# Kernel tuning notes

Measured on AMD Instinct MI355X. Metric: run time of the kernel, lower is better.

The kernel has to match this reference:

```python
import jax, jax.numpy as jnp
import numpy as np

N_EMBD = 1024
N_HEAD = 16
HEAD_DIM = N_EMBD // N_HEAD


def setup_inputs() -> dict:
    key = jax.random.key(0)
    ks = jax.random.split(key, 9)
    s = 1.0 / np.sqrt(N_EMBD)
    x = jax.random.normal(ks[0], (2, 2048, N_EMBD), dtype=jnp.float32)
    # PyTorch Linear weights stored as (out_features, in_features)
    Wq = jax.random.uniform(ks[1], (N_EMBD, N_EMBD), jnp.float32, -s, s)
    bq = jax.random.uniform(ks[2], (N_EMBD,), jnp.float32, -s, s)
    Wk = jax.random.uniform(ks[3], (N_EMBD, N_EMBD), jnp.float32, -s, s)
    bk = jax.random.uniform(ks[4], (N_EMBD,), jnp.float32, -s, s)
    Wv = jax.random.uniform(ks[5], (N_EMBD, N_EMBD), jnp.float32, -s, s)
    bv = jax.random.uniform(ks[6], (N_EMBD,), jnp.float32, -s, s)
    Wfc = jax.random.uniform(ks[7], (N_EMBD, N_EMBD), jnp.float32, -s, s)
    bfc = jax.random.uniform(ks[8], (N_EMBD,), jnp.float32, -s, s)
    return {"x": x, "Wq": Wq, "bq": bq, "Wk": Wk, "bk": bk,
            "Wv": Wv, "bv": bv, "Wfc": Wfc, "bfc": bfc}


def reference(x, Wq, bq, Wk, bk, Wv, bv, Wfc, bfc):
    B, S, _ = x.shape

    def proj(W, b):
        y = jnp.einsum('bsd,ed->bse', x, W) + b  # Linear: x @ W.T + b
        return y.reshape(B, S, N_HEAD, HEAD_DIM).transpose(0, 2, 1, 3)  # [B,H,S,Dh]

    q = proj(Wq, bq)
    k = proj(Wk, bk)
    v = proj(Wv, bv)
    scores = jnp.einsum('bhqd,bhkd->bhqk', q, k) / jnp.sqrt(jnp.float32(HEAD_DIM))
    weights = jax.nn.softmax(scores, axis=-1)  # [B,H,S,S]
    out = jnp.einsum('bhqk,bhkd->bhqd', weights, v)
    out = out.transpose(0, 2, 1, 3).reshape(B, S, N_EMBD)
    out = jnp.einsum('bsd,ed->bse', out, Wfc) + bfc
    return (out, weights)
```

## Files before the change

### kernel.cpp

```cpp
#include <hip/hip_runtime.h>
#include <hip/hip_bf16.h>
#include <stdint.h>


typedef __attribute__((ext_vector_type(8))) short bf16x8;
typedef __attribute__((ext_vector_type(4))) short bf16x4;
typedef __attribute__((ext_vector_type(4))) float f32x4;

#define MFMA16(a, b, c) __builtin_amdgcn_mfma_f32_16x16x32_bf16(a, b, c, 0, 0, 0)

__device__ __forceinline__ short f2bf(float x) {
  uint32_t u = __builtin_bit_cast(uint32_t, x);
  u += 0x7FFFu + ((u >> 16) & 1u);
  return (short)(u >> 16);
}

__device__ __forceinline__ uint32_t cvtpk_bf16(float lo, float hi) {
  uint32_t r;
  asm("v_cvt_pk_bf16_f32 %0, %1, %2" : "=v"(r) : "v"(lo), "v"(hi));
  return r;
}

__device__ __forceinline__ void gload16(const void* g, void* l) {
  __builtin_amdgcn_global_load_lds((const __attribute__((address_space(1))) uint32_t*)g,
                                   (__attribute__((address_space(3))) uint32_t*)l, 16, 0, 0);
}

__global__ __launch_bounds__(256) void cvt_k(const float* __restrict__ src,
                                             short* __restrict__ dst, int n4) {
  int i = blockIdx.x * 256 + threadIdx.x;
  if (i < n4) {
    f32x4 v = *(const f32x4*)(src + (size_t)i * 4);
    bf16x4 o;
    o[0] = f2bf(v[0]); o[1] = f2bf(v[1]); o[2] = f2bf(v[2]); o[3] = f2bf(v[3]);
    *(bf16x4*)(dst + (size_t)i * 4) = o;
  }
}

template <int EPI>
__global__ __launch_bounds__(256) void gemm_k(
    const short* __restrict__ A, const short* __restrict__ B,
    const float* __restrict__ bq, const float* __restrict__ bk,
    const float* __restrict__ bv,
    short* __restrict__ Qb, short* __restrict__ Kb, short* __restrict__ Vt,
    float* __restrict__ Fout) {
  const int K = 1024;
  __shared__ short sA[128 * 32];
  __shared__ short sB[128 * 32];
  const int tid = threadIdx.x;
  const int w = tid >> 6, lane = tid & 63;
  const int wr = w >> 1, wc = w & 1;
  const int lrow = lane & 15, lk = (lane >> 4) * 8;
  const int tileM = blockIdx.x * 128, tileN = blockIdx.y * 128;

  f32x4 acc[4][4];
#pragma unroll
  for (int i = 0; i < 4; ++i)
#pragma unroll
    for (int j = 0; j < 4; ++j) acc[i][j] = (f32x4){0.f, 0.f, 0.f, 0.f};

  for (int k0 = 0; k0 < K; k0 += 32) {
#pragma unroll
    for (int i = 0; i < 2; ++i) {
      int u = (w * 2 + i) * 64 + lane;
      int row = u >> 2, c8 = (u & 3) * 8;
      gload16(A + (size_t)(tileM + row) * K + k0 + c8, (short*)sA + (w * 2 + i) * 512);
      gload16(B + (size_t)(tileN + row) * K + k0 + c8, (short*)sB + (w * 2 + i) * 512);
    }
    __syncthreads();
    bf16x8 af[4], bfr[4];
#pragma unroll
    for (int mi = 0; mi < 4; ++mi)
      af[mi] = *(const bf16x8*)&sA[(wr * 64 + mi * 16 + lrow) * 32 + lk];
#pragma unroll
    for (int ni = 0; ni < 4; ++ni)
      bfr[ni] = *(const bf16x8*)&sB[(wc * 64 + ni * 16 + lrow) * 32 + lk];
#pragma unroll
    for (int mi = 0; mi < 4; ++mi)
#pragma unroll
      for (int ni = 0; ni < 4; ++ni)
        acc[mi][ni] = MFMA16(af[mi], bfr[ni], acc[mi][ni]);
    __syncthreads();
  }

#pragma unroll
  for (int mi = 0; mi < 4; ++mi) {
    int m0 = tileM + wr * 64 + mi * 16 + (lane >> 4) * 4;
#pragma unroll
    for (int ni = 0; ni < 4; ++ni) {
      int n = tileN + wc * 64 + ni * 16 + lrow;
      f32x4 v = acc[mi][ni];
      if (EPI == 0) {
        int which = n >> 10, e = n & 1023;
        int h = e >> 6, dh = e & 63;
        float bias = (which == 0 ? bq : which == 1 ? bk : bv)[e];
        int b = m0 >> 11, s0 = m0 & 2047;
        size_t hb = (size_t)(b * 16 + h);
        if (which == 2) {
          int kt2 = s0 >> 5, gl = (s0 >> 3) & 3, ni2 = dh >> 4, j = dh & 15;
          size_t base = (((hb * 64 + kt2) * 4 + ni2) * 64 + gl * 16 + j) * 8 + (s0 & 7);
          bf16x4 pk;
#pragma unroll
          for (int r = 0; r < 4; ++r) pk[r] = f2bf(v[r] + bias);
          *(bf16x4*)&Vt[base] = pk;
        } else {
          short* dst = (which == 0) ? Qb : Kb;
          int tile = s0 >> 4, h2 = dh >> 5, gl = (dh >> 3) & 3, ci = dh & 7;
          size_t base = (((hb * 128 + tile) * 2 + h2) * 64 + gl * 16 + (s0 & 15)) * 8 + ci;
#pragma unroll
          for (int r = 0; r < 4; ++r) dst[base + r * 8] = f2bf(v[r] + bias);
        }
      } else {
        float bias = bq[n];
#pragma unroll
        for (int r = 0; r < 4; ++r)
          Fout[(size_t)(m0 + r) * 1024 + n] = v[r] + bias;
      }
    }
  }
}

__device__ __forceinline__ void sw1_phase(bf16x8& pa, bf16x8& pb, int nxt,
    const short* __restrict__ Kf, int l8, const bf16x8& aQ0, const bf16x8& aQ1,
    float kscale, float& ls0, float& ls1, float& ls2, float& ls3) {
  const f32x4 zero = {0.f, 0.f, 0.f, 0.f};
  f32x4 s = MFMA16(pa, aQ0, zero);
  s = MFMA16(pb, aQ1, s);
  pa = *(const bf16x8*)&Kf[nxt * 1024 + l8];
  pb = *(const bf16x8*)&Kf[nxt * 1024 + 512 + l8];
  ls0 += exp2f(s[0] * kscale);
  ls1 += exp2f(s[1] * kscale);
  ls2 += exp2f(s[2] * kscale);
  ls3 += exp2f(s[3] * kscale);
}

__device__ __forceinline__ void sw2_phase(
    bf16x8& k00, bf16x8& k01, bf16x8& k10, bf16x8& k11,
    bf16x8& v0, bf16x8& v1, bf16x8& v2, bf16x8& v3,
    int kt2, int nxt, short* __restrict__ wl,
    const short* __restrict__ Kw, const short* __restrict__ Vw, int l8,
    const bf16x8& aQ0, const bf16x8& aQ1, float rl, float kscale,
    float* __restrict__ Wqp, int lrow, int g,
    f32x4& o0, f32x4& o1, f32x4& o2, f32x4& o3) {
  const f32x4 zero = {0.f, 0.f, 0.f, 0.f};
  f32x4 sa = MFMA16(k00, aQ0, zero);
  sa = MFMA16(k01, aQ1, sa);
  f32x4 sb = MFMA16(k10, aQ0, zero);
  sb = MFMA16(k11, aQ1, sb);
  const short* Ktn = &Kw[nxt * 2048];
  k00 = *(const bf16x8*)&Ktn[l8];
  k01 = *(const bf16x8*)&Ktn[512 + l8];
  k10 = *(const bf16x8*)&Ktn[1024 + l8];
  k11 = *(const bf16x8*)&Ktn[1536 + l8];
  f32x4 ea, eb;
#pragma unroll
  for (int r = 0; r < 4; ++r) ea[r] = exp2f(sa[r] * kscale) * rl;
#pragma unroll
  for (int r = 0; r < 4; ++r) eb[r] = exp2f(sb[r] * kscale) * rl;
  *(f32x4*)&Wqp[kt2 * 32] = ea;
  *(f32x4*)&Wqp[kt2 * 32 + 16] = eb;
  uint2 pa, pb;
  pa.x = cvtpk_bf16(ea[0], ea[1]);
  pa.y = cvtpk_bf16(ea[2], ea[3]);
  pb.x = cvtpk_bf16(eb[0], eb[1]);
  pb.y = cvtpk_bf16(eb[2], eb[3]);
  *(uint2*)&wl[lrow * 40 + g * 4] = pa;
  *(uint2*)&wl[lrow * 40 + 16 + g * 4] = pb;
  const bf16x8 aW = *(const bf16x8*)&wl[lrow * 40 + g * 8];
  o0 = MFMA16(aW, v0, o0);
  o1 = MFMA16(aW, v1, o1);
  o2 = MFMA16(aW, v2, o2);
  o3 = MFMA16(aW, v3, o3);
  const short* Vpn = &Vw[nxt * 2048];
  v0 = *(const bf16x8*)&Vpn[l8];
  v1 = *(const bf16x8*)&Vpn[512 + l8];
  v2 = *(const bf16x8*)&Vpn[1024 + l8];
  v3 = *(const bf16x8*)&Vpn[1536 + l8];
}

__global__ __launch_bounds__(256, 4) void attn_k(
    const short* __restrict__ Qb, const short* __restrict__ Kb,
    const short* __restrict__ Vt, float* __restrict__ Wout,
    short* __restrict__ attn) {
  __shared__ short Wlds[4][2][16 * 40];
  const int i = blockIdx.x;
  const int bh = ((i & 7) << 2) | ((i >> 3) & 3);
  const int qt = i >> 5;
  const int w = threadIdx.x >> 6, lane = threadIdx.x & 63;
  const int lrow = lane & 15, g = lane >> 4;
  const int qb = qt * 4 + w;
  const int l8 = lane * 8;
  const short* Qf = Qb + (size_t)(bh * 128 + qb) * 1024;
  const short* Kf = Kb + (size_t)bh * (128 * 1024);
  const short* Vf = Vt + (size_t)bh * (64 * 2048);
  const float kscale = 0.125f * 1.44269504088896f;
  const f32x4 zero = {0.f, 0.f, 0.f, 0.f};

  const bf16x8 aQ0 = *(const bf16x8*)&Qf[l8];
  const bf16x8 aQ1 = *(const bf16x8*)&Qf[512 + l8];

  float ls0 = 0.f, ls1 = 0.f, ls2 = 0.f, ls3 = 0.f;
  bf16x8 p0a = *(const bf16x8*)&Kf[0 * 1024 + l8];
  bf16x8 p0b = *(const bf16x8*)&Kf[0 * 1024 + 512 + l8];
  bf16x8 p1a = *(const bf16x8*)&Kf[1 * 1024 + l8];
  bf16x8 p1b = *(const bf16x8*)&Kf[1 * 1024 + 512 + l8];
  bf16x8 p2a = *(const bf16x8*)&Kf[2 * 1024 + l8];
  bf16x8 p2b = *(const bf16x8*)&Kf[2 * 1024 + 512 + l8];
  bf16x8 p3a = *(const bf16x8*)&Kf[3 * 1024 + l8];
  bf16x8 p3b = *(const bf16x8*)&Kf[3 * 1024 + 512 + l8];
  for (int kt = 0; kt < 128; kt += 4) {
    sw1_phase(p0a, p0b, (kt + 4) & 127, Kf, l8, aQ0, aQ1, kscale, ls0, ls1, ls2, ls3);
    sw1_phase(p1a, p1b, (kt + 5) & 127, Kf, l8, aQ0, aQ1, kscale, ls0, ls1, ls2, ls3);
    sw1_phase(p2a, p2b, (kt + 6) & 127, Kf, l8, aQ0, aQ1, kscale, ls0, ls1, ls2, ls3);
    sw1_phase(p3a, p3b, (kt + 7) & 127, Kf, l8, aQ0, aQ1, kscale, ls0, ls1, ls2, ls3);
  }
  float lsum = (ls0 + ls1) + (ls2 + ls3);
  lsum += __shfl_xor(lsum, 16);
  lsum += __shfl_xor(lsum, 32);
  const float rl = 1.0f / lsum;

  f32x4 o0 = zero, o1 = zero, o2 = zero, o3 = zero;
  float* Wqp = Wout + ((size_t)bh * 2048 + qb * 16 + lrow) * 2048 + g * 4;
  short* wlA = &Wlds[w][0][0];
  short* wlB = &Wlds[w][1][0];
  bf16x8 ka00 = *(const bf16x8*)&Kf[l8],        ka01 = *(const bf16x8*)&Kf[512 + l8];
  bf16x8 ka10 = *(const bf16x8*)&Kf[1024 + l8], ka11 = *(const bf16x8*)&Kf[1536 + l8];
  bf16x8 va0 = *(const bf16x8*)&Vf[l8],         va1 = *(const bf16x8*)&Vf[512 + l8];
  bf16x8 va2 = *(const bf16x8*)&Vf[1024 + l8],  va3 = *(const bf16x8*)&Vf[1536 + l8];
  bf16x8 kb00 = *(const bf16x8*)&Kf[2048 + l8], kb01 = *(const bf16x8*)&Kf[2560 + l8];
  bf16x8 kb10 = *(const bf16x8*)&Kf[3072 + l8], kb11 = *(const bf16x8*)&Kf[3584 + l8];
  bf16x8 vb0 = *(const bf16x8*)&Vf[2048 + l8],  vb1 = *(const bf16x8*)&Vf[2560 + l8];
  bf16x8 vb2 = *(const bf16x8*)&Vf[3072 + l8],  vb3 = *(const bf16x8*)&Vf[3584 + l8];
  for (int kt2 = 0; kt2 < 64; kt2 += 2) {
    sw2_phase(ka00, ka01, ka10, ka11, va0, va1, va2, va3,
              kt2, (kt2 + 2) & 63, wlA, Kf, Vf, l8, aQ0, aQ1, rl, kscale,
              Wqp, lrow, g, o0, o1, o2, o3);
    sw2_phase(kb00, kb01, kb10, kb11, vb0, vb1, vb2, vb3,
              kt2 + 1, (kt2 + 3) & 63, wlB, Kf, Vf, l8, aQ0, aQ1, rl, kscale,
              Wqp, lrow, g, o0, o1, o2, o3);
  }

  const int b = bh >> 4, h = bh & 15;
  const size_t obase = (size_t)(b * 2048 + qb * 16 + g * 4) * 1024 + h * 64 + lrow;
#pragma unroll
  for (int r = 0; r < 4; ++r) {
    attn[obase + (size_t)r * 1024 +  0] = f2bf(o0[r]);
    attn[obase + (size_t)r * 1024 + 16] = f2bf(o1[r]);
    attn[obase + (size_t)r * 1024 + 32] = f2bf(o2[r]);
    attn[obase + (size_t)r * 1024 + 48] = f2bf(o3[r]);
  }
}

extern "C" void kernel_launch(void* const* d_in, const int* in_sizes, int n_in,
                              void* d_out, int out_size, void* d_ws,
                              size_t ws_size, hipStream_t stream) {
  const float* x   = (const float*)d_in[0];
  const float* Wq  = (const float*)d_in[1];
  const float* bq  = (const float*)d_in[2];
  const float* Wk  = (const float*)d_in[3];
  const float* bk  = (const float*)d_in[4];
  const float* Wv  = (const float*)d_in[5];
  const float* bv  = (const float*)d_in[6];
  const float* Wfc = (const float*)d_in[7];
  const float* bfc = (const float*)d_in[8];

  float* out  = (float*)d_out;
  float* wout = out + (size_t)4194304;

  char* ws = (char*)d_ws;
  short* xb   = (short*)(ws);
  short* wqkv = (short*)(ws + ((size_t)8  << 20));
  short* wfcb = (short*)(ws + ((size_t)14 << 20));
  short* Qb   = (short*)(ws + ((size_t)16 << 20));
  short* Kb   = (short*)(ws + ((size_t)24 << 20));
  short* Vt   = (short*)(ws + ((size_t)32 << 20));
  short* attn = xb;

  cvt_k<<<4096, 256, 0, stream>>>(x, xb, 1048576);
  cvt_k<<<1024, 256, 0, stream>>>(Wq, wqkv, 262144);
  cvt_k<<<1024, 256, 0, stream>>>(Wk, wqkv + 1048576, 262144);
  cvt_k<<<1024, 256, 0, stream>>>(Wv, wqkv + 2097152, 262144);
  cvt_k<<<1024, 256, 0, stream>>>(Wfc, wfcb, 262144);

  gemm_k<0><<<dim3(32, 24), 256, 0, stream>>>(xb, wqkv, bq, bk, bv, Qb, Kb, Vt,
                                              (float*)nullptr);

  attn_k<<<dim3(1024), 256, 0, stream>>>(Qb, Kb, Vt, wout, attn);

  gemm_k<1><<<dim3(32, 8), 256, 0, stream>>>(attn, wfcb, bfc, nullptr, nullptr,
                                             nullptr, nullptr, nullptr, out);
}
```

Measured before the change: 271.5 us.

## Fuse weight conversions into one launch, use native exp2 and MFMA priority hints

Replaces four separate weight fp32-to-bf16 conversion launches with a single kernel that picks its source by block index, removing launch overhead. In the attention inner phases, exp2f is replaced by the hardware exp2 builtin to drop range-handling instructions. s_setprio is raised around MFMA groups to favour matrix-issue scheduling across waves. The native exp2 may differ slightly for denormal inputs.

After: 275.9 us. No clear change (+1.6%).

```diff
diff --git a/kernel.cpp b/kernel.cpp
--- a/kernel.cpp
+++ b/kernel.cpp
@@ -8,6 +8,7 @@
 typedef __attribute__((ext_vector_type(4))) float f32x4;
 
 #define MFMA16(a, b, c) __builtin_amdgcn_mfma_f32_16x16x32_bf16(a, b, c, 0, 0, 0)
+#define EXP2(x) __builtin_amdgcn_exp2f(x)
 
 __device__ __forceinline__ short f2bf(float x) {
   uint32_t u = __builtin_bit_cast(uint32_t, x);
@@ -35,6 +36,19 @@
     o[0] = f2bf(v[0]); o[1] = f2bf(v[1]); o[2] = f2bf(v[2]); o[3] = f2bf(v[3]);
     *(bf16x4*)(dst + (size_t)i * 4) = o;
   }
+}
+
+__global__ __launch_bounds__(256) void cvtw_k(
+    const float* __restrict__ w0, const float* __restrict__ w1,
+    const float* __restrict__ w2, const float* __restrict__ w3,
+    short* __restrict__ dst) {
+  const int which = blockIdx.x >> 10;
+  const float* src = which == 0 ? w0 : which == 1 ? w1 : which == 2 ? w2 : w3;
+  const int i = (blockIdx.x & 1023) * 256 + threadIdx.x;
+  f32x4 v = *(const f32x4*)(src + (size_t)i * 4);
+  bf16x4 o;
+  o[0] = f2bf(v[0]); o[1] = f2bf(v[1]); o[2] = f2bf(v[2]); o[3] = f2bf(v[3]);
+  *(bf16x4*)(dst + (size_t)which * 1048576 + (size_t)i * 4) = o;
 }
 
 template <int EPI>
@@ -124,14 +138,16 @@
     const short* __restrict__ Kf, int l8, const bf16x8& aQ0, const bf16x8& aQ1,
     float kscale, float& ls0, float& ls1, float& ls2, float& ls3) {
   const f32x4 zero = {0.f, 0.f, 0.f, 0.f};
+  __builtin_amdgcn_s_setprio(1);
   f32x4 s = MFMA16(pa, aQ0, zero);
   s = MFMA16(pb, aQ1, s);
+  __builtin_amdgcn_s_setprio(0);
   pa = *(const bf16x8*)&Kf[nxt * 1024 + l8];
   pb = *(const bf16x8*)&Kf[nxt * 1024 + 512 + l8];
-  ls0 += exp2f(s[0] * kscale);
-  ls1 += exp2f(s[1] * kscale);
-  ls2 += exp2f(s[2] * kscale);
-  ls3 += exp2f(s[3] * kscale);
+  ls0 += EXP2(s[0] * kscale);
+  ls1 += EXP2(s[1] * kscale);
+  ls2 += EXP2(s[2] * kscale);
+  ls3 += EXP2(s[3] * kscale);
 }
 
 __device__ __forceinline__ void sw2_phase(
@@ -143,10 +159,12 @@
     float* __restrict__ Wqp, int lrow, int g,
     f32x4& o0, f32x4& o1, f32x4& o2, f32x4& o3) {
   const f32x4 zero = {0.f, 0.f, 0.f, 0.f};
+  __builtin_amdgcn_s_setprio(1);
   f32x4 sa = MFMA16(k00, aQ0, zero);
   sa = MFMA16(k01, aQ1, sa);
   f32x4 sb = MFMA16(k10, aQ0, zero);
   sb = MFMA16(k11, aQ1, sb);
+  __builtin_amdgcn_s_setprio(0);
   const short* Ktn = &Kw[nxt * 2048];
   k00 = *(const bf16x8*)&Ktn[l8];
   k01 = *(const bf16x8*)&Ktn[512 + l8];
@@ -154,9 +172,9 @@
   k11 = *(const bf16x8*)&Ktn[1536 + l8];
   f32x4 ea, eb;
 #pragma unroll
-  for (int r = 0; r < 4; ++r) ea[r] = exp2f(sa[r] * kscale) * rl;
-#pragma unroll
-  for (int r = 0; r < 4; ++r) eb[r] = exp2f(sb[r] * kscale) * rl;
+  for (int r = 0; r < 4; ++r) ea[r] = EXP2(sa[r] * kscale) * rl;
+#pragma unroll
+  for (int r = 0; r < 4; ++r) eb[r] = EXP2(sb[r] * kscale) * rl;
   *(f32x4*)&Wqp[kt2 * 32] = ea;
   *(f32x4*)&Wqp[kt2 * 32 + 16] = eb;
   uint2 pa, pb;
@@ -167,10 +185,12 @@
   *(uint2*)&wl[lrow * 40 + g * 4] = pa;
   *(uint2*)&wl[lrow * 40 + 16 + g * 4] = pb;
   const bf16x8 aW = *(const bf16x8*)&wl[lrow * 40 + g * 8];
+  __builtin_amdgcn_s_setprio(1);
   o0 = MFMA16(aW, v0, o0);
   o1 = MFMA16(aW, v1, o1);
   o2 = MFMA16(aW, v2, o2);
   o3 = MFMA16(aW, v3, o3);
+  __builtin_amdgcn_s_setprio(0);
   const short* Vpn = &Vw[nxt * 2048];
   v0 = *(const bf16x8*)&Vpn[l8];
   v1 = *(const bf16x8*)&Vpn[512 + l8];
@@ -277,10 +297,7 @@
   short* attn = xb;
 
   cvt_k<<<4096, 256, 0, stream>>>(x, xb, 1048576);
-  cvt_k<<<1024, 256, 0, stream>>>(Wq, wqkv, 262144);
-  cvt_k<<<1024, 256, 0, stream>>>(Wk, wqkv + 1048576, 262144);
-  cvt_k<<<1024, 256, 0, stream>>>(Wv, wqkv + 2097152, 262144);
-  cvt_k<<<1024, 256, 0, stream>>>(Wfc, wfcb, 262144);
+  cvtw_k<<<4096, 256, 0, stream>>>(Wq, Wk, Wv, Wfc, wqkv);
 
   gemm_k<0><<<dim3(32, 24), 256, 0, stream>>>(xb, wqkv, bq, bk, bv, Qb, Kb, Vt,
                                               (float*)nullptr);
```
